# Optimization experiments

Measured on AMD Instinct MI355X. Metric: run time of the kernel, lower is better.

Reference implementation:

```python
import jax, jax.numpy as jnp
import numpy as np

GROUPS = 256   # B: number of index groups
SEQ = 512      # L: tokens per group (equal-length groups)
D_IN = 128
D_QK = 64
D_V = 128


def setup_inputs() -> dict:
    key = jax.random.key(0)
    ks = jax.random.split(key, 7)
    N = GROUPS * SEQ
    inputs = jax.random.normal(ks[0], (N, D_IN), dtype=jnp.float32)
    # sorted group ids: GROUPS groups of SEQ tokens each
    index = jnp.repeat(jnp.arange(GROUPS, dtype=jnp.int64), SEQ)
    s_in = 1.0 / np.sqrt(D_IN)
    Wq = jax.random.normal(ks[1], (D_IN, D_QK), dtype=jnp.float32) * s_in
    bq = jax.random.normal(ks[2], (D_QK,), dtype=jnp.float32) * 0.01
    Wk = jax.random.normal(ks[3], (D_IN, D_QK), dtype=jnp.float32) * s_in
    bk = jax.random.normal(ks[4], (D_QK,), dtype=jnp.float32) * 0.01
    Wv = jax.random.normal(ks[5], (D_IN, D_V), dtype=jnp.float32) * s_in
    bv = jax.random.normal(ks[6], (D_V,), dtype=jnp.float32) * 0.01
    return {"inputs": inputs, "index": index, "Wq": Wq, "bq": bq,
            "Wk": Wk, "bk": bk, "Wv": Wv, "bv": bv}


def reference(inputs, index, Wq, bq, Wk, bk, Wv, bv):
    # Linear projections on flat tokens [N, d]
    q = inputs @ Wq + bq          # [N, D_QK]
    k = inputs @ Wk + bk          # [N, D_QK]
    v = inputs @ Wv + bv          # [N, D_V]
    # unbatch: equal-length sorted groups -> [B, L, d]
    q = q.reshape(GROUPS, SEQ, D_QK)
    k = k.reshape(GROUPS, SEQ, D_QK)
    v = v.reshape(GROUPS, SEQ, D_V)
    # note the module's scale: sqrt(2 * d_qk)
    scale = 1.0 / np.sqrt(2.0 * D_QK).astype(np.float32)
    scores = jnp.einsum('bqd,bkd->bqk', q, k) * scale   # [B, L, L]
    attn = jax.nn.softmax(scores, axis=-1)
    out = jnp.einsum('bqk,bkd->bqd', attn, v)           # [B, L, D_V]
    return out.reshape(-1, D_V)                          # [N, D_V]
```

## Files before the change

### kernel.cpp

```cpp
#include <hip/hip_runtime.h>
#include <hip/hip_bf16.h>
#include <stdint.h>

#define GROUPS 256
#define SEQ    512
#define D_IN   128
#define D_QK   64
#define D_V    128
#define NTOK   (GROUPS * SEQ)

#define SL2E (0.08838834764831845f * 1.4426950408889634f)

typedef short bf8 __attribute__((ext_vector_type(8)));
typedef short bf4 __attribute__((ext_vector_type(4)));
typedef float f32x4 __attribute__((ext_vector_type(4)));

__device__ __forceinline__ short f2bf(float f) {
    __bf16 h = (__bf16)f;
    return __builtin_bit_cast(short, h);
}

__device__ __forceinline__ void gload_lds16(const void* g, void* l) {
    __builtin_amdgcn_global_load_lds(
        (const __attribute__((address_space(1))) unsigned int*)(uintptr_t)(g),
        (__attribute__((address_space(3))) unsigned int*)(uint32_t)(uintptr_t)(l),
        16, 0, 0);
}

__global__ __launch_bounds__(256) void prep_w(
    const float* __restrict__ Wq, const float* __restrict__ bq,
    const float* __restrict__ Wk, const float* __restrict__ bk,
    const float* __restrict__ Wv, const float* __restrict__ bv,
    short* __restrict__ Wt, float* __restrict__ bcat)
{
    const int t = blockIdx.x * 256 + threadIdx.x;
    const int r  = t >> 5;
    const int k0 = (t & 31) * 4;
    const float* W; int ld; int c; float sc;
    if (r < 64)       { W = Wq; ld = 64;  c = r;       sc = SL2E; }
    else if (r < 128) { W = Wk; ld = 64;  c = r - 64;  sc = 1.0f; }
    else              { W = Wv; ld = 128; c = r - 128; sc = 1.0f; }
    bf4 pk;
#pragma unroll
    for (int i = 0; i < 4; ++i) pk[i] = f2bf(W[(size_t)(k0 + i) * ld + c] * sc);
    const int phys = (k0 * 2) ^ ((r & 7) << 4);
    *reinterpret_cast<bf4*>((char*)Wt + r * 256 + phys) = pk;
    if (t < 256) {
        const float* b = (t < 64) ? bq : (t < 128 ? bk : bv);
        const int cb   = (t < 64) ? t  : (t < 128 ? t - 64 : t - 128);
        bcat[t] = b[cb] * (t < 64 ? SL2E : 1.0f);
    }
}

__global__ __launch_bounds__(256) void proj_kernel(
    const float* __restrict__ x, const short* __restrict__ Wt,
    const float* __restrict__ bcat,
    short* __restrict__ Q, short* __restrict__ K, short* __restrict__ Vt)
{
    __shared__ short wlds[16384];
    const int tid = threadIdx.x;
    const int wid = tid >> 6, lane = tid & 63, l15 = lane & 15, lg = lane >> 4;

#pragma unroll
    for (int i = 0; i < 8; ++i)
        gload_lds16((const char*)Wt + i * 4096 + tid * 16,
                    (char*)wlds + i * 4096 + tid * 16);

    const size_t tw = (size_t)blockIdx.x * 128 + wid * 32;
    const int g     = (int)(tw >> 9);
    const int tseg  = (int)(tw & 511);

    bf8 xf[2][4];
#pragma unroll
    for (int m = 0; m < 2; ++m) {
        const float* xr = x + (tw + m * 16 + l15) * D_IN;
#pragma unroll
        for (int kf = 0; kf < 4; ++kf) {
            const float4 a = *reinterpret_cast<const float4*>(xr + kf * 32 + lg * 8);
            const float4 b = *reinterpret_cast<const float4*>(xr + kf * 32 + lg * 8 + 4);
            bf8 v;
            v[0] = f2bf(a.x); v[1] = f2bf(a.y); v[2] = f2bf(a.z); v[3] = f2bf(a.w);
            v[4] = f2bf(b.x); v[5] = f2bf(b.y); v[6] = f2bf(b.z); v[7] = f2bf(b.w);
            xf[m][kf] = v;
        }
    }
    __syncthreads();

#pragma unroll
    for (int cf = 0; cf < 8; ++cf) {
        const int wrow = cf * 16 + l15;
        bf8 wf[4];
#pragma unroll
        for (int kf = 0; kf < 4; ++kf) {
            const int off = (kf * 64 + lg * 16) ^ ((wrow & 7) << 4);
            wf[kf] = *reinterpret_cast<const bf8*>((const char*)wlds + wrow * 256 + off);
        }
        const float4 bias4 = *reinterpret_cast<const float4*>(bcat + cf * 16 + lg * 4);
#pragma unroll
        for (int m = 0; m < 2; ++m) {
            f32x4 acc = (f32x4){0.f, 0.f, 0.f, 0.f};
#pragma unroll
            for (int kf = 0; kf < 4; ++kf)
                acc = __builtin_amdgcn_mfma_f32_16x16x32_bf16(wf[kf], xf[m][kf], acc, 0, 0, 0);
            bf4 pk;
            pk[0] = f2bf(acc[0] + bias4.x); pk[1] = f2bf(acc[1] + bias4.y);
            pk[2] = f2bf(acc[2] + bias4.z); pk[3] = f2bf(acc[3] + bias4.w);
            const size_t tok = tw + m * 16 + l15;
            if (cf < 4) {
                *reinterpret_cast<bf4*>((char*)Q + tok * 128 + cf * 32 + lg * 8) = pk;
            } else {
                const int lo = ((cf - 4) * 32 + lg * 8) ^ (((int)tok & 7) << 4);
                *reinterpret_cast<bf4*>((char*)K + tok * 128 + lo) = pk;
            }
        }
    }
    __syncthreads();

#pragma unroll
    for (int i = 0; i < 8; ++i)
        gload_lds16((const char*)Wt + 32768 + i * 4096 + tid * 16,
                    (char*)wlds + i * 4096 + tid * 16);
    __syncthreads();

#pragma unroll
    for (int cf = 8; cf < 16; ++cf) {
        const int lrow = (cf - 8) * 16 + l15;
        bf8 wf[4];
#pragma unroll
        for (int kf = 0; kf < 4; ++kf) {
            const int off = (kf * 64 + lg * 16) ^ ((lrow & 7) << 4);
            wf[kf] = *reinterpret_cast<const bf8*>((const char*)wlds + lrow * 256 + off);
        }
        const int d = (cf - 8) * 16 + l15;
        const float bias = bcat[cf * 16 + l15];
        const int sd = (d >> 1) & 3;
        char* vg = (char*)Vt + (size_t)g * 131072 + (size_t)d * 64;
#pragma unroll
        for (int m = 0; m < 2; ++m) {
            f32x4 acc = (f32x4){0.f, 0.f, 0.f, 0.f};
#pragma unroll
            for (int kf = 0; kf < 4; ++kf)
                acc = __builtin_amdgcn_mfma_f32_16x16x32_bf16(xf[m][kf], wf[kf], acc, 0, 0, 0);
            bf4 pk;
#pragma unroll
            for (int r = 0; r < 4; ++r) pk[r] = f2bf(acc[r] + bias);
            const int t0    = tseg + m * 16;
            const int inner = ((lg ^ sd) << 4) + ((t0 >> 4) & 1) * 8;
            *reinterpret_cast<bf4*>(vg + (size_t)(t0 >> 5) * 8192 + inner) = pk;
        }
    }
}

__global__ __launch_bounds__(256, 4) void attn_kernel(
    const short* __restrict__ Q, const short* __restrict__ K,
    const short* __restrict__ Vt, float* __restrict__ out)
{
    __shared__ short lds[2 * 6144];
    const int id  = blockIdx.x;
    const int xcd = id & 7;
    const int j   = id >> 3;
    const int g   = xcd * 32 + (j >> 2);
    const int rb  = j & 3;
    const int tid = threadIdx.x, wid = tid >> 6, lane = tid & 63;
    const int l15 = lane & 15, lg = lane >> 4;
    const size_t gtok = (size_t)g * SEQ;
    const int row0 = rb * 128 + wid * 32;

    bf8 qf[2][2];
#pragma unroll
    for (int rf = 0; rf < 2; ++rf) {
        const short* qr = Q + (gtok + row0 + rf * 16 + l15) * 64 + lg * 8;
        qf[rf][0] = *reinterpret_cast<const bf8*>(qr);
        qf[rf][1] = *reinterpret_cast<const bf8*>(qr + 32);
    }

    const char* Kg = (const char*)(K + gtok * 64);
    const char* Vg = (const char*)Vt + (size_t)g * 131072;

    f32x4 o[2][8];
#pragma unroll
    for (int rf = 0; rf < 2; ++rf)
#pragma unroll
        for (int vt = 0; vt < 8; ++vt) o[rf][vt] = (f32x4){0.f, 0.f, 0.f, 0.f};
    f32x4 psv[2] = {(f32x4){0.f, 0.f, 0.f, 0.f}, (f32x4){0.f, 0.f, 0.f, 0.f}};
    const bf8 onesf = {0x3F80, 0x3F80, 0x3F80, 0x3F80, 0x3F80, 0x3F80, 0x3F80, 0x3F80};

    auto stage = [&](int kt, int b) {
        char* lbase = (char*)lds + b * 12288;
        int c = wid * 3;
#pragma unroll
        for (int i = 0; i < 3; ++i, ++c) {
            if (c < 4) {
                gload_lds16(Kg + (size_t)kt * 4096 + c * 1024 + lane * 16,
                            lbase + c * 1024 + lane * 16);
            } else {
                gload_lds16(Vg + (size_t)kt * 8192 + (c - 4) * 1024 + lane * 16,
                            lbase + c * 1024 + lane * 16);
            }
        }
    };

    auto compute = [&](int b) {
        const char* lb = (const char*)lds + b * 12288;
        __builtin_amdgcn_s_setprio(1);
        f32x4 st[2][2];
#pragma unroll
        for (int tf = 0; tf < 2; ++tf) {
            const int tok = tf * 16 + l15;
            const char* kb = lb + tok * 128;
            const int x7 = (tok & 7) << 4;
            const bf8 k0 = *reinterpret_cast<const bf8*>(kb + ((lg * 16) ^ x7));
            const bf8 k1 = *reinterpret_cast<const bf8*>(kb + ((64 + lg * 16) ^ x7));
#pragma unroll
            for (int rf = 0; rf < 2; ++rf) {
                f32x4 s = (f32x4){0.f, 0.f, 0.f, 0.f};
                s = __builtin_amdgcn_mfma_f32_16x16x32_bf16(k0, qf[rf][0], s, 0, 0, 0);
                s = __builtin_amdgcn_mfma_f32_16x16x32_bf16(k1, qf[rf][1], s, 0, 0, 0);
                st[tf][rf] = s;
            }
        }
        bf8 pa[2];
#pragma unroll
        for (int rf = 0; rf < 2; ++rf) {
            bf8 pv;
#pragma unroll
            for (int i = 0; i < 4; ++i) {
                pv[i]     = f2bf(__builtin_amdgcn_exp2f(st[0][rf][i]));
                pv[i + 4] = f2bf(__builtin_amdgcn_exp2f(st[1][rf][i]));
            }
            pa[rf] = pv;
            psv[rf] = __builtin_amdgcn_mfma_f32_16x16x32_bf16(pv, onesf, psv[rf], 0, 0, 0);
        }
        const char* vb = lb + 4096;
#pragma unroll
        for (int vt = 0; vt < 8; ++vt) {
            const int d = vt * 16 + l15;
            const char* vr = vb + d * 64;
            const bf8 v0 = *reinterpret_cast<const bf8*>(vr + ((lg * 16) ^ ((((d >> 1) & 3)) << 4)));
            o[0][vt] = __builtin_amdgcn_mfma_f32_16x16x32_bf16(pa[0], v0, o[0][vt], 0, 0, 0);
            o[1][vt] = __builtin_amdgcn_mfma_f32_16x16x32_bf16(pa[1], v0, o[1][vt], 0, 0, 0);
        }
        __builtin_amdgcn_s_setprio(0);
    };

    stage(0, 0);
    __syncthreads();
    for (int kt = 0; kt < 16; ++kt) {
        const int b = kt & 1;
        if (kt < 15) stage(kt + 1, b ^ 1);
        compute(b);
        __syncthreads();
    }

#pragma unroll
    for (int rf = 0; rf < 2; ++rf) {
        float linv[4];
#pragma unroll
        for (int r = 0; r < 4; ++r) linv[r] = 1.0f / psv[rf][r];
        float* op = out + (gtok + row0 + rf * 16) * D_V;
#pragma unroll
        for (int vt = 0; vt < 8; ++vt)
#pragma unroll
            for (int r = 0; r < 4; ++r)
                op[(size_t)(lg * 4 + r) * D_V + vt * 16 + l15] = o[rf][vt][r] * linv[r];
    }
}

extern "C" void kernel_launch(void* const* d_in, const int* in_sizes, int n_in,
                              void* d_out, int out_size, void* d_ws, size_t ws_size,
                              hipStream_t stream) {
    (void)in_sizes; (void)n_in; (void)ws_size; (void)out_size;
    const float* x  = (const float*)d_in[0];
    const float* Wq = (const float*)d_in[2];
    const float* bq = (const float*)d_in[3];
    const float* Wk = (const float*)d_in[4];
    const float* bk = (const float*)d_in[5];
    const float* Wv = (const float*)d_in[6];
    const float* bv = (const float*)d_in[7];
    float* out = (float*)d_out;

    short* Qw = (short*)d_ws;
    short* Kw = Qw + (size_t)NTOK * D_QK;
    short* Vt = Kw + (size_t)NTOK * D_QK;

    short* Wt   = (short*)out;
    float* bcat = (float*)((char*)out + 65536);

    prep_w<<<32, 256, 0, stream>>>(Wq, bq, Wk, bk, Wv, bv, Wt, bcat);
    proj_kernel<<<NTOK / 128, 256, 0, stream>>>(x, Wt, bcat, Qw, Kw, Vt);
    attn_kernel<<<1024, 256, 0, stream>>>(Qw, Kw, Vt, out);
}
```

Before: 65.76 us.

## Switch Q/K/V intermediates to quad-planar layouts matching the MFMA fragment order

Stores Q, K and V^T in planar layouts where each group of four bf16 values sits in its own plane. Writes from the projection kernel become contiguous 8-byte stores, and the attention kernel reads fragments with two 8-byte LDS or global loads per operand. This replaces the earlier XOR-swizzled 16-byte layouts, with the aim of removing bank conflicts and scattered stores in the projection epilogue. The cost is twice as many, narrower LDS reads in the attention inner loop, and strided global reads of Q across planes.

```diff
diff --git a/kernel.cpp b/kernel.cpp
--- a/kernel.cpp
+++ b/kernel.cpp
@@ -18,6 +18,10 @@
 __device__ __forceinline__ short f2bf(float f) {
     __bf16 h = (__bf16)f;
     return __builtin_bit_cast(short, h);
+}
+
+__device__ __forceinline__ bf8 cat8(bf4 a, bf4 b) {
+    return __builtin_shufflevector(a, b, 0, 1, 2, 3, 4, 5, 6, 7);
 }
 
 __device__ __forceinline__ void gload_lds16(const void* g, void* l) {
@@ -55,7 +59,7 @@
 __global__ __launch_bounds__(256) void proj_kernel(
     const float* __restrict__ x, const short* __restrict__ Wt,
     const float* __restrict__ bcat,
-    short* __restrict__ Q, short* __restrict__ K, short* __restrict__ Vt)
+    char* __restrict__ Q, char* __restrict__ K, char* __restrict__ Vt)
 {
     __shared__ short wlds[16384];
     const int tid = threadIdx.x;
@@ -107,10 +111,12 @@
             pk[2] = f2bf(acc[2] + bias4.z); pk[3] = f2bf(acc[3] + bias4.w);
             const size_t tok = tw + m * 16 + l15;
             if (cf < 4) {
-                *reinterpret_cast<bf4*>((char*)Q + tok * 128 + cf * 32 + lg * 8) = pk;
+                const size_t p = (size_t)(cf * 4 + lg);
+                *reinterpret_cast<bf4*>(Q + (p * NTOK + tok) * 8) = pk;
             } else {
-                const int lo = ((cf - 4) * 32 + lg * 8) ^ (((int)tok & 7) << 4);
-                *reinterpret_cast<bf4*>((char*)K + tok * 128 + lo) = pk;
+                const size_t gt = tok >> 5;
+                const int    p  = (cf - 4) * 4 + lg;
+                *reinterpret_cast<bf4*>(K + gt * 4096 + p * 256 + (tok & 31) * 8) = pk;
             }
         }
     }
@@ -133,8 +139,6 @@
         }
         const int d = (cf - 8) * 16 + l15;
         const float bias = bcat[cf * 16 + l15];
-        const int sd = (d >> 1) & 3;
-        char* vg = (char*)Vt + (size_t)g * 131072 + (size_t)d * 64;
 #pragma unroll
         for (int m = 0; m < 2; ++m) {
             f32x4 acc = (f32x4){0.f, 0.f, 0.f, 0.f};
@@ -144,18 +148,19 @@
             bf4 pk;
 #pragma unroll
             for (int r = 0; r < 4; ++r) pk[r] = f2bf(acc[r] + bias);
-            const int t0    = tseg + m * 16;
-            const int inner = ((lg ^ sd) << 4) + ((t0 >> 4) & 1) * 8;
-            *reinterpret_cast<bf4*>(vg + (size_t)(t0 >> 5) * 8192 + inner) = pk;
+            const int t0     = tseg + m * 16;
+            const size_t gt  = (size_t)g * 16 + (t0 >> 5);
+            const int    qd  = ((t0 >> 4) & 1) * 4 + lg;
+            *reinterpret_cast<bf4*>(Vt + gt * 8192 + qd * 1024 + d * 8) = pk;
         }
     }
 }
 
 __global__ __launch_bounds__(256, 4) void attn_kernel(
-    const short* __restrict__ Q, const short* __restrict__ K,
-    const short* __restrict__ Vt, float* __restrict__ out)
+    const char* __restrict__ Q, const char* __restrict__ K,
+    const char* __restrict__ Vt, float* __restrict__ out)
 {
-    __shared__ short lds[2 * 6144];
+    __shared__ char lds[2 * 12288];
     const int id  = blockIdx.x;
     const int xcd = id & 7;
     const int j   = id >> 3;
@@ -169,13 +174,17 @@
     bf8 qf[2][2];
 #pragma unroll
     for (int rf = 0; rf < 2; ++rf) {
-        const short* qr = Q + (gtok + row0 + rf * 16 + l15) * 64 + lg * 8;
-        qf[rf][0] = *reinterpret_cast<const bf8*>(qr);
-        qf[rf][1] = *reinterpret_cast<const bf8*>(qr + 32);
-    }
-
-    const char* Kg = (const char*)(K + gtok * 64);
-    const char* Vg = (const char*)Vt + (size_t)g * 131072;
+        const size_t tq = gtok + row0 + rf * 16 + l15;
+        const bf4 a0 = *reinterpret_cast<const bf4*>(Q + ((size_t)(2 * lg)     * NTOK + tq) * 8);
+        const bf4 a1 = *reinterpret_cast<const bf4*>(Q + ((size_t)(2 * lg + 1) * NTOK + tq) * 8);
+        const bf4 b0 = *reinterpret_cast<const bf4*>(Q + ((size_t)(8 + 2 * lg) * NTOK + tq) * 8);
+        const bf4 b1 = *reinterpret_cast<const bf4*>(Q + ((size_t)(9 + 2 * lg) * NTOK + tq) * 8);
+        qf[rf][0] = cat8(a0, a1);
+        qf[rf][1] = cat8(b0, b1);
+    }
+
+    const char* Kg = K + (size_t)g * 16 * 4096;
+    const char* Vg = Vt + (size_t)g * 16 * 8192;
 
     f32x4 o[2][8];
 #pragma unroll
@@ -207,10 +216,12 @@
 #pragma unroll
         for (int tf = 0; tf < 2; ++tf) {
             const int tok = tf * 16 + l15;
-            const char* kb = lb + tok * 128;
-            const int x7 = (tok & 7) << 4;
-            const bf8 k0 = *reinterpret_cast<const bf8*>(kb + ((lg * 16) ^ x7));
-            const bf8 k1 = *reinterpret_cast<const bf8*>(kb + ((64 + lg * 16) ^ x7));
+            const bf4 ka0 = *reinterpret_cast<const bf4*>(lb + (2 * lg)     * 256 + tok * 8);
+            const bf4 ka1 = *reinterpret_cast<const bf4*>(lb + (2 * lg + 1) * 256 + tok * 8);
+            const bf4 kb0 = *reinterpret_cast<const bf4*>(lb + (8 + 2 * lg) * 256 + tok * 8);
+            const bf4 kb1 = *reinterpret_cast<const bf4*>(lb + (9 + 2 * lg) * 256 + tok * 8);
+            const bf8 k0 = cat8(ka0, ka1);
+            const bf8 k1 = cat8(kb0, kb1);
 #pragma unroll
             for (int rf = 0; rf < 2; ++rf) {
                 f32x4 s = (f32x4){0.f, 0.f, 0.f, 0.f};
@@ -235,8 +246,9 @@
 #pragma unroll
         for (int vt = 0; vt < 8; ++vt) {
             const int d = vt * 16 + l15;
-            const char* vr = vb + d * 64;
-            const bf8 v0 = *reinterpret_cast<const bf8*>(vr + ((lg * 16) ^ ((((d >> 1) & 3)) << 4)));
+            const bf4 va = *reinterpret_cast<const bf4*>(vb + lg * 1024 + d * 8);
+            const bf4 vbq = *reinterpret_cast<const bf4*>(vb + (4 + lg) * 1024 + d * 8);
+            const bf8 v0 = cat8(va, vbq);
             o[0][vt] = __builtin_amdgcn_mfma_f32_16x16x32_bf16(pa[0], v0, o[0][vt], 0, 0, 0);
             o[1][vt] = __builtin_amdgcn_mfma_f32_16x16x32_bf16(pa[1], v0, o[1][vt], 0, 0, 0);
         }
@@ -279,9 +291,9 @@
     const float* bv = (const float*)d_in[7];
     float* out = (float*)d_out;
 
-    short* Qw = (short*)d_ws;
-    short* Kw = Qw + (size_t)NTOK * D_QK;
-    short* Vt = Kw + (size_t)NTOK * D_QK;
+    char* Qw = (char*)d_ws;
+    char* Kw = Qw + (size_t)NTOK * 64 * 2;
+    char* Vt = Kw + (size_t)NTOK * 64 * 2;
 
     short* Wt   = (short*)out;
     float* bcat = (float*)((char*)out + 65536);
```

Measured after the change: 66.20 us. About the same (+0.7%).
